# Kernel tuning notes

Hardware: AMD Instinct MI355X
Metric: run time of the kernel (lower is better)

## Reference

```python
import jax, jax.numpy as jnp
import numpy as np

SIGMA = 0.5
TAU = 2.0
S = (128, 128, 128)
C = 16
B = 32


def _make_grid():
    ax = [jnp.arange(s, dtype=jnp.float32) for s in S]
    g = jnp.stack(jnp.meshgrid(*ax, indexing='ij'), axis=-1)  # [X,Y,Z,3]
    return g.reshape(-1, 3)  # [N,3]


def setup_inputs() -> dict:
    key = jax.random.key(0)
    k1, k2, k3 = jax.random.split(key, 3)
    N = S[0] * S[1] * S[2]
    memory = jax.random.normal(k1, (N, C), dtype=jnp.float32) * 0.02
    grid = _make_grid()
    ray_origin = jax.random.uniform(k2, (B, 3), dtype=jnp.float32) * 127.0
    d = jax.random.normal(k3, (B, 3), dtype=jnp.float32)
    ray_dir = d / jnp.linalg.norm(d, axis=-1, keepdims=True)
    return {"memory": memory, "grid": grid, "ray_origin": ray_origin, "ray_dir": ray_dir}


def reference(memory, grid, ray_origin, ray_dir):
    # read(): per-ray Gaussian-tube kernel over the full grid, weighted sum of memory.
    # lax.map over rays keeps peak intermediates at [N,3] instead of [B,N,3] (1.5 GB).
    def one(od):
        o, d = od
        dx = grid - o                      # [N,3]
        t = dx @ d                         # [N]  projection parameter
        x_proj = o + t[:, None] * d        # [N,3]
        r2 = jnp.sum((grid - x_proj) ** 2, axis=-1)  # [N] squared dist to ray
        k = jnp.exp(-r2 / (2.0 * SIGMA ** 2)) * jnp.exp(-jnp.maximum(t, 0.0) / TAU)
        return k @ memory                  # [C]
    return jax.lax.map(one, (ray_origin, ray_dir))  # [B,C]
```

## Files before the change

kernel.cpp:

```cpp
#include <hip/hip_runtime.h>
#include <math.h>

namespace {

constexpr int kC = 16;
constexpr int kB = 32;
constexpr int kSlabs = 128;
constexpr int kS1Blocks = kB * kSlabs / 4;
constexpr int kSlotsPerRay = kSlabs / 4;

__global__ __launch_bounds__(256)
void hpm_stage1(const float* __restrict__ memory,
                const float* __restrict__ ray_o,
                const float* __restrict__ ray_d,
                float* __restrict__ ws)
{
    __shared__ float part[4][kC];

    const int b    = (int)blockIdx.x;
    const int ray  = b >> 5;
    const int sg   = b & 31;
    const int w    = (int)(threadIdx.x >> 6);
    const int lane = (int)(threadIdx.x & 63);
    const int slab = sg * 4 + w;

    const float ox = ray_o[3 * ray + 0], oy = ray_o[3 * ray + 1], oz = ray_o[3 * ray + 2];
    const float dx = ray_d[3 * ray + 0], dy = ray_d[3 * ray + 1], dz = ray_d[3 * ray + 2];

    const float adx = fabsf(dx), ady = fabsf(dy), adz = fabsf(dz);
    int a0;
    if (adx >= ady && adx >= adz) a0 = 0; else if (ady >= adz) a0 = 1; else a0 = 2;
    const float o0 = (a0 == 0) ? ox : ((a0 == 1) ? oy : oz);
    const float d0 = (a0 == 0) ? dx : ((a0 == 1) ? dy : dz);
    const float o1 = (a0 == 0) ? oy : ox;
    const float d1 = (a0 == 0) ? dy : dx;
    const float o2 = (a0 == 2) ? oy : oz;
    const float d2 = (a0 == 2) ? dy : dz;
    const int st0 = (a0 == 0) ? 16384 : ((a0 == 1) ? 128 : 1);
    const int st1 = (a0 == 0) ? 128 : 16384;
    const int st2 = (a0 == 2) ? 128 : 1;

    const float sa  = (float)slab;
    const float t_s = (sa - o0) / d0;
    const float c1  = fmaf(t_s, d1, o1);
    const float c2  = fmaf(t_s, d2, o2);

    const bool slab_ok = (fmaxf(t_s, 0.0f) < 38.5f) &&
                         (c1 > -5.5f) && (c1 < 132.5f) &&
                         (c2 > -5.5f) && (c2 < 132.5f);

    float a[kC];
    #pragma unroll
    for (int i = 0; i < kC; ++i) a[i] = 0.0f;
    bool hit = false;

    if (slab_ok) {
        const int r1  = (int)rintf(c1);
        const int r2i = (int)rintf(c2);
        const float4* __restrict__ mem4 = reinterpret_cast<const float4*>(memory);
        #pragma unroll
        for (int cc = 0; cc < 2; ++cc) {
            const int q = lane + cc * 64;
            if (q < 121) {
                const int y = r1  + (q / 11) - 5;
                const int z = r2i + (q % 11) - 5;
                if ((unsigned)y < 128u && (unsigned)z < 128u) {
                    const float e0 = sa - o0;
                    const float e1 = (float)y - o1;
                    const float e2 = (float)z - o2;
                    const float t  = fmaf(e0, d0, fmaf(e1, d1, e2 * d2));
                    const float g0 = fmaf(-t, d0, e0);
                    const float g1 = fmaf(-t, d1, e1);
                    const float g2 = fmaf(-t, d2, e2);
                    const float rr = fmaf(g0, g0, fmaf(g1, g1, g2 * g2));
                    const float arg = fmaf(-2.0f, rr, -0.5f * fmaxf(t, 0.0f));
                    if (arg > -16.0f) {
                        const float k = __expf(arg);
                        const int idx = slab * st0 + y * st1 + z * st2;
                        const float4 m0 = mem4[idx * 4 + 0];
                        const float4 m1 = mem4[idx * 4 + 1];
                        const float4 m2 = mem4[idx * 4 + 2];
                        const float4 m3 = mem4[idx * 4 + 3];
                        a[ 0] = fmaf(k, m0.x, a[ 0]); a[ 1] = fmaf(k, m0.y, a[ 1]);
                        a[ 2] = fmaf(k, m0.z, a[ 2]); a[ 3] = fmaf(k, m0.w, a[ 3]);
                        a[ 4] = fmaf(k, m1.x, a[ 4]); a[ 5] = fmaf(k, m1.y, a[ 5]);
                        a[ 6] = fmaf(k, m1.z, a[ 6]); a[ 7] = fmaf(k, m1.w, a[ 7]);
                        a[ 8] = fmaf(k, m2.x, a[ 8]); a[ 9] = fmaf(k, m2.y, a[ 9]);
                        a[10] = fmaf(k, m2.z, a[10]); a[11] = fmaf(k, m2.w, a[11]);
                        a[12] = fmaf(k, m3.x, a[12]); a[13] = fmaf(k, m3.y, a[13]);
                        a[14] = fmaf(k, m3.z, a[14]); a[15] = fmaf(k, m3.w, a[15]);
                        hit = true;
                    }
                }
            }
        }
    }

    if (__ballot(hit) != 0ull) {
        #pragma unroll
        for (int c = 0; c < kC; ++c) {
            float v = a[c];
            v += __shfl_xor(v,  1); v += __shfl_xor(v,  2);
            v += __shfl_xor(v,  4); v += __shfl_xor(v,  8);
            v += __shfl_xor(v, 16); v += __shfl_xor(v, 32);
            a[c] = v;
        }
    }
    if (lane == 0) {
        #pragma unroll
        for (int c = 0; c < kC; ++c) part[w][c] = a[c];
    }
    __syncthreads();

    if (threadIdx.x < kC) {
        const int c = (int)threadIdx.x;
        ws[b * kC + c] = (part[0][c] + part[1][c]) + (part[2][c] + part[3][c]);
    }
}

__global__ __launch_bounds__(256)
void hpm_stage2(const float* __restrict__ ws, float* __restrict__ out)
{
    __shared__ float red[16][kC + 1];
    const int ray = (int)blockIdx.x;
    const int t = (int)threadIdx.x;
    const int g = t >> 4;
    const int c = t & 15;
    const float* __restrict__ p = ws + (ray * kSlotsPerRay + g * 2) * kC + c;
    red[g][c] = p[0] + p[kC];
    __syncthreads();
    if (t < kC) {
        float s2 = 0.0f;
        #pragma unroll
        for (int w = 0; w < 16; ++w) s2 += red[w][t];
        out[ray * kC + t] = s2;
    }
}

}

extern "C" void kernel_launch(void* const* d_in, const int* in_sizes, int n_in,
                              void* d_out, int out_size, void* d_ws, size_t ws_size,
                              hipStream_t stream) {
    const float* memory = (const float*)d_in[0];
    const float* ray_o  = (const float*)d_in[2];
    const float* ray_d  = (const float*)d_in[3];
    float* out = (float*)d_out;
    float* ws  = (float*)d_ws;

    hpm_stage1<<<kS1Blocks, 256, 0, stream>>>(memory, ray_o, ray_d, ws);
    hpm_stage2<<<kB, 256, 0, stream>>>(ws, out);
}
```

Before: 13.24 us.

## Process four slabs per wave and use transpose-style butterfly wave reduction

Each wave now loops over four slabs instead of one, cutting the stage-1 grid from 1024 blocks to 256. Each wave writes its own partial directly, which removes the shared-memory block reduction and the __syncthreads. The 16-channel wave reduction now uses a recursive-halving butterfly, so each step exchanges half the remaining values, replacing 96 shuffles with about 17. The risk is less parallelism and less latency hiding from fewer blocks, while serial per-wave work grows.

```diff
diff --git a/kernel.cpp b/kernel.cpp
--- a/kernel.cpp
+++ b/kernel.cpp
@@ -6,8 +6,9 @@
 constexpr int kC = 16;
 constexpr int kB = 32;
 constexpr int kSlabs = 128;
-constexpr int kS1Blocks = kB * kSlabs / 4;
-constexpr int kSlotsPerRay = kSlabs / 4;
+constexpr int kSlabsPerWave = 4;
+constexpr int kWavesPerRay = kSlabs / kSlabsPerWave;
+constexpr int kS1Blocks = kB * kWavesPerRay / 4;
 
 __global__ __launch_bounds__(256)
 void hpm_stage1(const float* __restrict__ memory,
@@ -15,14 +16,19 @@
                 const float* __restrict__ ray_d,
                 float* __restrict__ ws)
 {
-    __shared__ float part[4][kC];
+    const int b    = (int)blockIdx.x;
+    const int ray  = b >> 3;
+    const int wid  = (int)(threadIdx.x >> 6);
+    const int lane = (int)(threadIdx.x & 63);
+    const int wir  = (b & 7) * 4 + wid;
+    const int slabbase = wir * kSlabsPerWave;
+    const int slot = b * 4 + wid;
 
-    const int b    = (int)blockIdx.x;
-    const int ray  = b >> 5;
-    const int sg   = b & 31;
-    const int w    = (int)(threadIdx.x >> 6);
-    const int lane = (int)(threadIdx.x & 63);
-    const int slab = sg * 4 + w;
+    const int q0 = lane;
+    const int q1 = lane + 64;
+    const bool qv1 = (q1 < 121);
+    const int o1a = q0 / 11 - 5, o2a = q0 % 11 - 5;
+    const int o1b = q1 / 11 - 5, o2b = q1 % 11 - 5;
 
     const float ox = ray_o[3 * ray + 0], oy = ray_o[3 * ray + 1], oz = ray_o[3 * ray + 2];
     const float dx = ray_d[3 * ray + 0], dy = ray_d[3 * ray + 1], dz = ray_d[3 * ray + 2];
@@ -39,82 +45,96 @@
     const int st0 = (a0 == 0) ? 16384 : ((a0 == 1) ? 128 : 1);
     const int st1 = (a0 == 0) ? 128 : 16384;
     const int st2 = (a0 == 2) ? 128 : 1;
+    const float inv_d0 = 1.0f / d0;
 
-    const float sa  = (float)slab;
-    const float t_s = (sa - o0) / d0;
-    const float c1  = fmaf(t_s, d1, o1);
-    const float c2  = fmaf(t_s, d2, o2);
-
-    const bool slab_ok = (fmaxf(t_s, 0.0f) < 38.5f) &&
-                         (c1 > -5.5f) && (c1 < 132.5f) &&
-                         (c2 > -5.5f) && (c2 < 132.5f);
+    const float4* __restrict__ mem4 = reinterpret_cast<const float4*>(memory);
 
     float a[kC];
     #pragma unroll
     for (int i = 0; i < kC; ++i) a[i] = 0.0f;
-    bool hit = false;
 
-    if (slab_ok) {
+    #pragma unroll
+    for (int j = 0; j < kSlabsPerWave; ++j) {
+        const int slab = slabbase + j;
+        const float sa  = (float)slab;
+        const float t_s = (sa - o0) * inv_d0;
+        const float c1  = fmaf(t_s, d1, o1);
+        const float c2  = fmaf(t_s, d2, o2);
+
+        const bool slab_ok = (fmaxf(t_s, 0.0f) < 38.5f) &&
+                             (c1 > -5.5f) && (c1 < 132.5f) &&
+                             (c2 > -5.5f) && (c2 < 132.5f);
+        if (!slab_ok) continue;
+
         const int r1  = (int)rintf(c1);
         const int r2i = (int)rintf(c2);
-        const float4* __restrict__ mem4 = reinterpret_cast<const float4*>(memory);
+        const float e0 = sa - o0;
+
         #pragma unroll
         for (int cc = 0; cc < 2; ++cc) {
-            const int q = lane + cc * 64;
-            if (q < 121) {
-                const int y = r1  + (q / 11) - 5;
-                const int z = r2i + (q % 11) - 5;
-                if ((unsigned)y < 128u && (unsigned)z < 128u) {
-                    const float e0 = sa - o0;
-                    const float e1 = (float)y - o1;
-                    const float e2 = (float)z - o2;
-                    const float t  = fmaf(e0, d0, fmaf(e1, d1, e2 * d2));
-                    const float g0 = fmaf(-t, d0, e0);
-                    const float g1 = fmaf(-t, d1, e1);
-                    const float g2 = fmaf(-t, d2, e2);
-                    const float rr = fmaf(g0, g0, fmaf(g1, g1, g2 * g2));
-                    const float arg = fmaf(-2.0f, rr, -0.5f * fmaxf(t, 0.0f));
-                    if (arg > -16.0f) {
-                        const float k = __expf(arg);
-                        const int idx = slab * st0 + y * st1 + z * st2;
-                        const float4 m0 = mem4[idx * 4 + 0];
-                        const float4 m1 = mem4[idx * 4 + 1];
-                        const float4 m2 = mem4[idx * 4 + 2];
-                        const float4 m3 = mem4[idx * 4 + 3];
-                        a[ 0] = fmaf(k, m0.x, a[ 0]); a[ 1] = fmaf(k, m0.y, a[ 1]);
-                        a[ 2] = fmaf(k, m0.z, a[ 2]); a[ 3] = fmaf(k, m0.w, a[ 3]);
-                        a[ 4] = fmaf(k, m1.x, a[ 4]); a[ 5] = fmaf(k, m1.y, a[ 5]);
-                        a[ 6] = fmaf(k, m1.z, a[ 6]); a[ 7] = fmaf(k, m1.w, a[ 7]);
-                        a[ 8] = fmaf(k, m2.x, a[ 8]); a[ 9] = fmaf(k, m2.y, a[ 9]);
-                        a[10] = fmaf(k, m2.z, a[10]); a[11] = fmaf(k, m2.w, a[11]);
-                        a[12] = fmaf(k, m3.x, a[12]); a[13] = fmaf(k, m3.y, a[13]);
-                        a[14] = fmaf(k, m3.z, a[14]); a[15] = fmaf(k, m3.w, a[15]);
-                        hit = true;
-                    }
+            if (cc == 1 && !qv1) continue;
+            const int y = r1  + (cc ? o1b : o1a);
+            const int z = r2i + (cc ? o2b : o2a);
+            if ((unsigned)y < 128u && (unsigned)z < 128u) {
+                const float e1 = (float)y - o1;
+                const float e2 = (float)z - o2;
+                const float t  = fmaf(e0, d0, fmaf(e1, d1, e2 * d2));
+                const float g0 = fmaf(-t, d0, e0);
+                const float g1 = fmaf(-t, d1, e1);
+                const float g2 = fmaf(-t, d2, e2);
+                const float rr = fmaf(g0, g0, fmaf(g1, g1, g2 * g2));
+                const float arg = fmaf(-2.0f, rr, -0.5f * fmaxf(t, 0.0f));
+                if (arg > -16.0f) {
+                    const float k = __expf(arg);
+                    const int idx = slab * st0 + y * st1 + z * st2;
+                    const float4 m0 = mem4[idx * 4 + 0];
+                    const float4 m1 = mem4[idx * 4 + 1];
+                    const float4 m2 = mem4[idx * 4 + 2];
+                    const float4 m3 = mem4[idx * 4 + 3];
+                    a[ 0] = fmaf(k, m0.x, a[ 0]); a[ 1] = fmaf(k, m0.y, a[ 1]);
+                    a[ 2] = fmaf(k, m0.z, a[ 2]); a[ 3] = fmaf(k, m0.w, a[ 3]);
+                    a[ 4] = fmaf(k, m1.x, a[ 4]); a[ 5] = fmaf(k, m1.y, a[ 5]);
+                    a[ 6] = fmaf(k, m1.z, a[ 6]); a[ 7] = fmaf(k, m1.w, a[ 7]);
+                    a[ 8] = fmaf(k, m2.x, a[ 8]); a[ 9] = fmaf(k, m2.y, a[ 9]);
+                    a[10] = fmaf(k, m2.z, a[10]); a[11] = fmaf(k, m2.w, a[11]);
+                    a[12] = fmaf(k, m3.x, a[12]); a[13] = fmaf(k, m3.y, a[13]);
+                    a[14] = fmaf(k, m3.z, a[14]); a[15] = fmaf(k, m3.w, a[15]);
                 }
             }
         }
     }
 
-    if (__ballot(hit) != 0ull) {
+    {
         #pragma unroll
-        for (int c = 0; c < kC; ++c) {
-            float v = a[c];
-            v += __shfl_xor(v,  1); v += __shfl_xor(v,  2);
-            v += __shfl_xor(v,  4); v += __shfl_xor(v,  8);
-            v += __shfl_xor(v, 16); v += __shfl_xor(v, 32);
-            a[c] = v;
+        for (int i = 0; i < 8; ++i) {
+            const float send = (lane & 1) ? a[i]     : a[i + 8];
+            const float keep = (lane & 1) ? a[i + 8] : a[i];
+            a[i] = keep + __shfl_xor(send, 1);
         }
+        #pragma unroll
+        for (int i = 0; i < 4; ++i) {
+            const float send = (lane & 2) ? a[i]     : a[i + 4];
+            const float keep = (lane & 2) ? a[i + 4] : a[i];
+            a[i] = keep + __shfl_xor(send, 2);
+        }
+        #pragma unroll
+        for (int i = 0; i < 2; ++i) {
+            const float send = (lane & 4) ? a[i]     : a[i + 2];
+            const float keep = (lane & 4) ? a[i + 2] : a[i];
+            a[i] = keep + __shfl_xor(send, 4);
+        }
+        {
+            const float send = (lane & 8) ? a[0] : a[1];
+            const float keep = (lane & 8) ? a[1] : a[0];
+            a[0] = keep + __shfl_xor(send, 8);
+        }
+        a[0] += __shfl_xor(a[0], 16);
+        a[0] += __shfl_xor(a[0], 32);
     }
-    if (lane == 0) {
-        #pragma unroll
-        for (int c = 0; c < kC; ++c) part[w][c] = a[c];
-    }
-    __syncthreads();
-
-    if (threadIdx.x < kC) {
-        const int c = (int)threadIdx.x;
-        ws[b * kC + c] = (part[0][c] + part[1][c]) + (part[2][c] + part[3][c]);
+    if (lane < 16) {
+        const int c = ((lane & 1) << 3) | ((lane & 2) << 1) |
+                      ((lane & 4) >> 1) | ((lane & 8) >> 3);
+        ws[slot * kC + c] = a[0];
     }
 }
 
@@ -126,7 +146,7 @@
     const int t = (int)threadIdx.x;
     const int g = t >> 4;
     const int c = t & 15;
-    const float* __restrict__ p = ws + (ray * kSlotsPerRay + g * 2) * kC + c;
+    const float* __restrict__ p = ws + (ray * kWavesPerRay + g * 2) * kC + c;
     red[g][c] = p[0] + p[kC];
     __syncthreads();
     if (t < kC) {
```

Result: faster. 11.57 us, median of 2 (-12.6%).
